# Optimization experiments

Measured on AMD Instinct MI355X. Metric: run time of the kernel, lower is better.

## Reference

```python
import jax, jax.numpy as jnp
import numpy as np


def _conv1x1(x, w, b=None):
    # x: (B, Cin, H, W), w: (Cout, Cin)
    y = jnp.einsum('oi,bihw->bohw', w, x)
    if b is not None:
        y = y + b[None, :, None, None]
    return y


def _adaptive_avg_pool(x, ps):
    # faithful torch AdaptiveAvgPool2d: bin i covers [floor(i*H/ps), ceil((i+1)*H/ps))
    H, W = x.shape[-2], x.shape[-1]
    rows = []
    for i in range(ps):
        hs, he = (i * H) // ps, -((-(i + 1) * H) // ps)
        cols = []
        for j in range(ps):
            ws, we = (j * W) // ps, -((-(j + 1) * W) // ps)
            cols.append(x[..., hs:he, ws:we].mean((-2, -1)))
        rows.append(jnp.stack(cols, -1))
    return jnp.stack(rows, -2)


def _bilinear(x, oh, ow, align_corners):
    H, W = x.shape[-2], x.shape[-1]
    def coords(o, I):
        if align_corners:
            c = jnp.arange(o, dtype=jnp.float32) * (float(I - 1) / max(o - 1, 1))
        else:
            c = jnp.clip((jnp.arange(o, dtype=jnp.float32) + 0.5) * (float(I) / o) - 0.5, 0.0, float(I - 1))
        i0 = jnp.floor(c).astype(jnp.int32)
        i1 = jnp.minimum(i0 + 1, I - 1)
        return i0, i1, (c - i0).astype(x.dtype)
    y0, y1, wy = coords(oh, H)
    x0, x1, wx = coords(ow, W)
    top = x[..., y0, :]
    bot = x[..., y1, :]
    a, b = top[..., x0], top[..., x1]
    c, d = bot[..., x0], bot[..., x1]
    r0 = a * (1 - wx) + b * wx
    r1 = c * (1 - wx) + d * wx
    return r0 * (1 - wy[:, None]) + r1 * wy[:, None]


def setup_inputs() -> dict:
    key = jax.random.key(0)
    ks = jax.random.split(key, 32)
    Cin, C, B, H, W = 512, 64, 2, 48, 48
    def rnd(k, shape, s=0.05):
        return jax.random.normal(k, shape, jnp.float32) * s
    inp = {
        'x': jax.random.normal(ks[0], (B, Cin, H, W), jnp.float32),
        'w_gc0': rnd(ks[1], (C, Cin)), 'b_gc0': rnd(ks[2], (C,)),
        'w_gc1': rnd(ks[3], (C, Cin)), 'b_gc1': rnd(ks[4], (C,)),
        'w_gc2': rnd(ks[5], (C, Cin)), 'b_gc2': rnd(ks[6], (C,)),
        'w_gc3': rnd(ks[7], (C, Cin)), 'b_gc3': rnd(ks[8], (C,)),
        'w_q': rnd(ks[9], (C // 8, C)), 'b_q': rnd(ks[10], (C // 8,)),
        'w_k': rnd(ks[11], (C // 8, C)), 'b_k': rnd(ks[12], (C // 8,)),
        'w_v': rnd(ks[13], (C, C)), 'b_v': rnd(ks[14], (C,)),
        'gamma': jnp.ones((1,), jnp.float32),
        'w_se1': rnd(ks[15], (C, C)), 'w_se2': rnd(ks[16], (C, C)),
        'w_se3': rnd(ks[17], (C, C)), 'w_se4': rnd(ks[18], (C, C)),
        'w_out0': rnd(ks[19], (256, 4 * C)), 'b_out0': rnd(ks[20], (256,)),
        'w_out1': rnd(ks[21], (128, 4 * C)), 'b_out1': rnd(ks[22], (128,)),
        'w_out2': rnd(ks[23], (64, 4 * C)), 'b_out2': rnd(ks[24], (64,)),
        'w_out3': rnd(ks[25], (64, 4 * C)), 'b_out3': rnd(ks[26], (64,)),
    }
    return inp


def reference(x, w_gc0, b_gc0, w_gc1, b_gc1, w_gc2, b_gc2, w_gc3, b_gc3,
              w_q, b_q, w_k, b_k, w_v, b_v, gamma,
              w_se1, w_se2, w_se3, w_se4,
              w_out0, b_out0, w_out1, b_out1, w_out2, b_out2, w_out3, b_out3):
    B, _, H, W = x.shape
    # multi-scale pooled branches (pool sizes 1,3,5), bilinear up w/ align_corners=True
    gcs = []
    for ps, w_, b_ in ((1, w_gc0, b_gc0), (3, w_gc1, b_gc1), (5, w_gc2, b_gc2)):
        p = jax.nn.relu(_conv1x1(_adaptive_avg_pool(x, ps), w_, b_))
        gcs.append(_bilinear(p, H, W, True))
    # full-resolution SA branch
    s = jax.nn.relu(_conv1x1(x, w_gc3, b_gc3))
    N = H * W
    q = _conv1x1(s, w_q, b_q).reshape(B, -1, N)   # (B, C/8, N)
    k = _conv1x1(s, w_k, b_k).reshape(B, -1, N)
    v = _conv1x1(s, w_v, b_v).reshape(B, -1, N)   # (B, C, N)
    attn = jax.nn.softmax(jnp.einsum('bcm,bcn->bmn', q, k), axis=-1)  # (B, N, N)
    sa = jnp.einsum('bcn,bmn->bcm', v, attn).reshape(s.shape)
    sa = gamma * sa + s
    # SE channel-attention weights (note original's cross pairing of branches)
    gap = lambda t: t.mean((2, 3), keepdims=True)
    y3 = _conv1x1(gap(gcs[0]), w_se4)
    y2 = _conv1x1(gap(gcs[1]), w_se3)
    y1 = _conv1x1(gap(gcs[2]), w_se2)
    y0 = _conv1x1(gap(sa), w_se1)
    wgt = jnp.concatenate([y0, y1, y2, y3], axis=2)      # (B, 64, 4, 1)
    wgt = jax.nn.softmax(jax.nn.sigmoid(wgt), axis=2)
    fused = jnp.concatenate([
        wgt[:, :, 0:1, :] * gcs[0],
        wgt[:, :, 1:2, :] * gcs[1],
        wgt[:, :, 2:3, :] * gcs[2],
        wgt[:, :, 3:4, :] * sa,
    ], axis=1)                                            # (B, 256, H, W)
    outs = []
    for sc, w_, b_ in ((2, w_out0, b_out0), (4, w_out1, b_out1), (8, w_out2, b_out2), (16, w_out3, b_out3)):
        y = jax.nn.relu(_conv1x1(fused, w_, b_))
        outs.append(_bilinear(y, H * sc, W * sc, False))  # nn.Upsample default align_corners=False
    return tuple(outs)
```

## Files before the change

### kernel.cpp

```cpp
#include <hip/hip_runtime.h>
#include <hip/hip_bf16.h>
#include <hip/hip_fp16.h>


typedef __attribute__((ext_vector_type(8))) short short8;
typedef __attribute__((ext_vector_type(4))) float f32x4;

#define GLOAD_LDS(gsrc, ldst) \
  __builtin_amdgcn_global_load_lds((const __attribute__((address_space(1))) void*)(gsrc), \
                                   (__attribute__((address_space(3))) void*)(ldst), 16, 0, 0)

static constexpr size_t OFF_P1 = 0;
static constexpr size_t OFF_P3 = OFF_P1 + 2*512;
static constexpr size_t OFF_P5 = OFF_P3 + 18*512;
static constexpr size_t OFF_G0 = OFF_P5 + 50*512;
static constexpr size_t OFF_G1 = OFF_G0 + 2*64;
static constexpr size_t OFF_G2 = OFF_G1 + 18*64;
static constexpr size_t OFF_S  = OFF_G2 + 50*64;
static constexpr size_t OFF_Q  = OFF_S  + 294912;
static constexpr size_t OFF_K  = OFF_Q  + 36864;
static constexpr size_t OFF_V  = OFF_K  + 36864;
static constexpr size_t OFF_SA = OFF_V  + 294912;
static constexpr size_t OFF_GC = OFF_SA + 294912;
static constexpr size_t OFF_MEAN = OFF_GC + 3*294912;
static constexpr size_t OFF_WGT  = OFF_MEAN + 512;
static constexpr size_t OFF_Y0 = OFF_WGT + 512;
static constexpr size_t OFF_Y1 = OFF_Y0 + 1179648;
static constexpr size_t OFF_Y2 = OFF_Y1 + 589824;
static constexpr size_t OFF_Y3 = OFF_Y2 + 294912;

__global__ __launch_bounds__(256) void k_pool(const float* __restrict__ x, float* __restrict__ wsp){
  __shared__ float pl[2304];
  __shared__ float red[4];
  int bc = blockIdx.x;
  int b = bc >> 9, cin = bc & 511;
  const float* src = x + (size_t)bc * 2304;
  int t = threadIdx.x;
  float ls = 0.f;
  #pragma unroll
  for (int j = 0; j < 9; j++){ int i = t + j*256; float v = src[i]; pl[i] = v; ls += v; }
  #pragma unroll
  for (int o = 32; o; o >>= 1) ls += __shfl_xor(ls, o);
  if ((t & 63) == 0) red[t >> 6] = ls;
  __syncthreads();
  if (t == 0) wsp[OFF_P1 + (size_t)b*512 + cin] = (red[0]+red[1]+red[2]+red[3]) * (1.f/2304.f);
  if (t < 9){
    int ry = t/3, rx = t%3; float sm = 0.f;
    for (int yy = 0; yy < 16; yy++)
      for (int xx = 0; xx < 16; xx++) sm += pl[(ry*16+yy)*48 + rx*16+xx];
    wsp[OFF_P3 + ((size_t)b*9 + t)*512 + cin] = sm * (1.f/256.f);
  } else if (t < 34){
    int j = t - 9; int ry = j/5, rx = j%5;
    int hs = (ry*48)/5, he = ((ry+1)*48+4)/5, cs = (rx*48)/5, ce = ((rx+1)*48+4)/5;
    float sm = 0.f;
    for (int yy = hs; yy < he; yy++)
      for (int xx = cs; xx < ce; xx++) sm += pl[yy*48+xx];
    wsp[OFF_P5 + ((size_t)b*25 + j)*512 + cin] = sm / (float)((he-hs)*(ce-cs));
  }
}

__global__ __launch_bounds__(256) void k_gcconv(
    const float* __restrict__ w0, const float* __restrict__ b0,
    const float* __restrict__ w1, const float* __restrict__ b1,
    const float* __restrict__ w2, const float* __restrict__ b2,
    float* __restrict__ wsp){
  int col = blockIdx.x;
  const float* w; const float* bias; const float* pool; float* dst;
  if (col < 2){ w = w0; bias = b0; pool = wsp + OFF_P1 + (size_t)col*512; dst = wsp + OFF_G0 + (size_t)col*64; }
  else if (col < 20){ int c = col-2;  w = w1; bias = b1; pool = wsp + OFF_P3 + (size_t)c*512; dst = wsp + OFF_G1 + (size_t)c*64; }
  else              { int c = col-20; w = w2; bias = b2; pool = wsp + OFF_P5 + (size_t)c*512; dst = wsp + OFF_G2 + (size_t)c*64; }
  int t = threadIdx.x; int r = t >> 2, qd = t & 3;
  const float* wr = w + (size_t)r*512 + qd*128;
  const float* pr = pool + qd*128;
  float acc = 0.f;
  #pragma unroll 8
  for (int k = 0; k < 128; k += 4){
    float4 wv = *(const float4*)(wr + k); float4 pv = *(const float4*)(pr + k);
    acc += wv.x*pv.x + wv.y*pv.y + wv.z*pv.z + wv.w*pv.w;
  }
  acc += __shfl_xor(acc, 1); acc += __shfl_xor(acc, 2);
  if (qd == 0) dst[r] = fmaxf(acc + bias[r], 0.f);
}

__global__ __launch_bounds__(256) void k_sgemm_qkv(const float* __restrict__ x,
    const float* __restrict__ w, const float* __restrict__ bias,
    const float* __restrict__ wq, const float* __restrict__ bq,
    const float* __restrict__ wk, const float* __restrict__ bk,
    const float* __restrict__ wv, const float* __restrict__ bv,
    float* __restrict__ wsp){
  __shared__ __align__(16) float wt[64][66];
  __shared__ __align__(16) float xs[64][32];
  __shared__ __align__(16) float s_lds[64][36];
  __shared__ float wq_lds[80][64];
  __shared__ float bqkv[80];
  int cb = blockIdx.x;
  int b = cb / 72, hw0 = (cb - b*72)*32;
  int tid = threadIdx.x;
  int wv_ = tid >> 6, lane = tid & 63;
  for (int i = tid; i < 5120; i += 256){
    int row = i >> 6, k = i & 63;
    wq_lds[row][k] = (row < 8) ? wq[(size_t)row*64 + k]
                   : (row < 16) ? wk[(size_t)(row-8)*64 + k]
                                : wv[(size_t)(row-16)*64 + k];
  }
  if (tid < 80) bqkv[tid] = (tid < 8) ? bq[tid] : (tid < 16) ? bk[tid-8] : bv[tid-16];
  int sr = tid >> 2, sseg = tid & 3;
  int cc0 = (tid & 7)*4, r0 = (tid >> 3)*2;
  const float* xb = x + (size_t)b*512*2304 + hw0;
  float acc[2][4] = {};
  for (int kc = 0; kc < 512; kc += 64){
    __syncthreads();
    {
      int rr0 = wv_*16 + (lane >> 3);
      const float* g0 = xb + (size_t)(kc + rr0)*2304 + (lane & 7)*4;
      const float* g1 = xb + (size_t)(kc + rr0 + 8)*2304 + (lane & 7)*4;
      GLOAD_LDS(g0, &xs[wv_*16][0]);
      GLOAD_LDS(g1, &xs[wv_*16 + 8][0]);
    }
    #pragma unroll
    for (int i = 0; i < 16; i += 4){
      float4 v = *(const float4*)(w + (size_t)sr*512 + kc + sseg*16 + i);
      wt[sseg*16+i+0][sr]=v.x; wt[sseg*16+i+1][sr]=v.y;
      wt[sseg*16+i+2][sr]=v.z; wt[sseg*16+i+3][sr]=v.w;
    }
    __syncthreads();
    #pragma unroll 4
    for (int k = 0; k < 64; k++){
      float2 wv2 = *(const float2*)&wt[k][r0];
      float4 xv = *(const float4*)&xs[k][cc0];
      acc[0][0]+=wv2.x*xv.x; acc[0][1]+=wv2.x*xv.y; acc[0][2]+=wv2.x*xv.z; acc[0][3]+=wv2.x*xv.w;
      acc[1][0]+=wv2.y*xv.x; acc[1][1]+=wv2.y*xv.y; acc[1][2]+=wv2.y*xv.z; acc[1][3]+=wv2.y*xv.w;
    }
  }
  #pragma unroll
  for (int i = 0; i < 2; i++){
    float bi = bias[r0+i];
    float4 o;
    o.x = fmaxf(acc[i][0]+bi, 0.f); o.y = fmaxf(acc[i][1]+bi, 0.f);
    o.z = fmaxf(acc[i][2]+bi, 0.f); o.w = fmaxf(acc[i][3]+bi, 0.f);
    *(float4*)(wsp + OFF_S + ((size_t)b*64 + r0+i)*2304 + hw0 + cc0) = o;
    *(float4*)&s_lds[r0+i][cc0] = o;
  }
  __syncthreads();
  int col = tid & 31, rgrp = tid >> 5;
  float a2[10];
  #pragma unroll
  for (int i = 0; i < 10; i++) a2[i] = bqkv[rgrp*10 + i];
  for (int k = 0; k < 64; k++){
    float sv = s_lds[k][col];
    #pragma unroll
    for (int i = 0; i < 10; i++) a2[i] += wq_lds[rgrp*10 + i][k]*sv;
  }
  __hip_bfloat16* Vb = reinterpret_cast<__hip_bfloat16*>(wsp + OFF_V);
  int hw = hw0 + col;
  #pragma unroll
  for (int i = 0; i < 10; i++){
    int r = rgrp*10 + i;
    if (r < 8)       wsp[OFF_Q + (size_t)b*18432 + (size_t)r*2304 + hw] = a2[i];
    else if (r < 16) wsp[OFF_K + (size_t)b*18432 + (size_t)(r-8)*2304 + hw] = a2[i];
    else             Vb[(size_t)b*147456 + (size_t)(r-16)*2304 + hw] = __float2bfloat16(a2[i]);
  }
}

__global__ __launch_bounds__(256) void k_attn(float* __restrict__ wsp, const float* __restrict__ gamma){
  int mb = blockIdx.x * 16;
  int b  = blockIdx.y;
  int t = threadIdx.x;
  int w = t >> 6, lane = t & 63;
  int arow = lane & 15, kg = lane >> 4;
  __shared__ float qs[16][8];
  __shared__ __align__(16) unsigned short plds[16][2312];
  __shared__ float redM[4][16], redS[4][16];
  __shared__ float tile[16][68];
  const float* Qp = wsp + OFF_Q + (size_t)b*18432;
  const float* Kp = wsp + OFF_K + (size_t)b*18432;
  if (t < 128) qs[t>>3][t&7] = Qp[(size_t)(t&7)*2304 + mb + (t>>3)];
  __syncthreads();
  float k8[9][8];
  #pragma unroll
  for (int j = 0; j < 9; j++){
    int n = j*256 + t;
    #pragma unroll
    for (int c = 0; c < 8; c++) k8[j][c] = Kp[(size_t)c*2304 + n];
  }
  float mx[16], ssum[16];
  #pragma unroll
  for (int m = 0; m < 16; m++){
    float q0=qs[m][0], q1=qs[m][1], q2=qs[m][2], q3=qs[m][3];
    float q4=qs[m][4], q5=qs[m][5], q6=qs[m][6], q7=qs[m][7];
    float lmx = -1e30f, ls = 0.f;
    #pragma unroll
    for (int j = 0; j < 9; j++){
      float l = q0*k8[j][0]+q1*k8[j][1]+q2*k8[j][2]+q3*k8[j][3]
              + q4*k8[j][4]+q5*k8[j][5]+q6*k8[j][6]+q7*k8[j][7];
      __half hv = __float2half(l);
      plds[m][j*256 + t] = __half_as_ushort(hv);
      float mo = lmx;
      lmx = fmaxf(lmx, l);
      ls = ls*__expf(mo - lmx) + __expf(l - lmx);
    }
    mx[m] = lmx; ssum[m] = ls;
  }
  #pragma unroll
  for (int m = 0; m < 16; m++){
    float M = mx[m], S = ssum[m];
    #pragma unroll
    for (int off = 32; off; off >>= 1){
      float oM = __shfl_xor(M, off), oS = __shfl_xor(S, off);
      float nM = fmaxf(M, oM);
      S = S*__expf(M - nM) + oS*__expf(oM - nM);
      M = nM;
    }
    if (lane == 0){ redM[w][m] = M; redS[w][m] = S; }
  }
  __syncthreads();
  float Mf[16], invS[16];
  #pragma unroll
  for (int m = 0; m < 16; m++){
    float M0 = redM[0][m], M1 = redM[1][m], M2 = redM[2][m], M3 = redM[3][m];
    float M = fmaxf(fmaxf(M0, M1), fmaxf(M2, M3));
    float S = redS[0][m]*__expf(M0-M) + redS[1][m]*__expf(M1-M)
            + redS[2][m]*__expf(M2-M) + redS[3][m]*__expf(M3-M);
    Mf[m] = M; invS[m] = 1.f/S;
  }
  const short* Vb = (const short*)(wsp + OFF_V) + (size_t)b*147456 + (size_t)(w*16 + arow)*2304;
  f32x4 acc = {0.f, 0.f, 0.f, 0.f};
  for (int j = 0; j < 9; j++){
    int n = j*256 + t;
    #pragma unroll
    for (int m = 0; m < 16; m++){
      float l = __half2float(__ushort_as_half(plds[m][n]));
      float p = __expf(l - Mf[m]) * invS[m];
      __hip_bfloat16 pb = __float2bfloat16(p);
      plds[m][n] = *(unsigned short*)&pb;
    }
    __syncthreads();
    #pragma unroll
    for (int ks = 0; ks < 8; ks++){
      int nb = j*256 + ks*32 + kg*8;
      short8 a  = *(const short8*)&plds[arow][nb];
      short8 bv = *(const short8*)(Vb + nb);
      acc = __builtin_amdgcn_mfma_f32_16x16x32_bf16(a, bv, acc, 0, 0, 0);
    }
  }
  #pragma unroll
  for (int r = 0; r < 4; r++) tile[kg*4 + r][w*16 + arow] = acc[r];
  __syncthreads();
  int c = t >> 2, mq = t & 3;
  float g = gamma[0];
  const float* Sp = wsp + OFF_S + (size_t)b*147456 + (size_t)c*2304 + mb + mq*4;
  float4 s4 = *(const float4*)Sp;
  float4 o;
  o.x = g*tile[mq*4+0][c] + s4.x;
  o.y = g*tile[mq*4+1][c] + s4.y;
  o.z = g*tile[mq*4+2][c] + s4.z;
  o.w = g*tile[mq*4+3][c] + s4.w;
  *(float4*)(wsp + OFF_SA + (size_t)b*147456 + (size_t)c*2304 + mb + mq*4) = o;
}

__device__ void gcup_body(int u, float* __restrict__ wsp){
  int px = (u % 9)*256 + threadIdx.x;
  int pb = u / 9;
  int c = pb & 63, b = (pb >> 6) & 1, t = pb >> 7;
  int oy = px / 48, ox = px - oy*48;
  int ps; const float* g;
  if (t == 0){ ps = 1; g = wsp + OFF_G0 + (size_t)b*64; }
  else if (t == 1){ ps = 3; g = wsp + OFF_G1 + (size_t)b*9*64; }
  else { ps = 5; g = wsp + OFF_G2 + (size_t)b*25*64; }
  float scale = (ps - 1) / 47.f;
  float cy = oy*scale, cx = ox*scale;
  int y0 = (int)cy, x0 = (int)cx;
  float wy = cy - y0, wx = cx - x0;
  int y1 = min(y0+1, ps-1), x1 = min(x0+1, ps-1);
  float a  = g[(y0*ps+x0)*64 + c], bq = g[(y0*ps+x1)*64 + c];
  float cc = g[(y1*ps+x0)*64 + c], d  = g[(y1*ps+x1)*64 + c];
  float v = (a*(1.f-wx) + bq*wx)*(1.f-wy) + (cc*(1.f-wx) + d*wx)*wy;
  wsp[OFF_GC + (((size_t)t*2 + b)*64 + c)*2304 + px] = v;
}

__device__ void gap_body(int blk, float* __restrict__ wsp){
  __shared__ float red[4];
  int c = blk & 63, b = blk >> 6;
  const float* src = wsp + OFF_SA + ((size_t)b*64 + c)*2304;
  float s = 0.f;
  for (int i = threadIdx.x; i < 2304; i += 256) s += src[i];
  #pragma unroll
  for (int o = 32; o; o >>= 1) s += __shfl_xor(s, o);
  if ((threadIdx.x & 63) == 0) red[threadIdx.x >> 6] = s;
  __syncthreads();
  if (threadIdx.x == 0)
    wsp[OFF_MEAN + (size_t)b*64 + c] = (red[0]+red[1]+red[2]+red[3]) * (1.f/2304.f);
}

__global__ __launch_bounds__(256) void k_gcup_gap(float* __restrict__ wsp){
  int bx = blockIdx.x;
  if (bx < 3456) gcup_body(bx, wsp);
  else           gap_body(bx - 3456, wsp);
}

__global__ __launch_bounds__(256) void k_se(
    const float* __restrict__ w_se1, const float* __restrict__ w_se2,
    const float* __restrict__ w_se3, const float* __restrict__ w_se4,
    float* __restrict__ wsp){
  int b = blockIdx.x; int tid = threadIdx.x;
  int g = tid >> 6, c = tid & 63;
  __shared__ float mean_lds[4][64];
  float mv;
  if (g == 0){
    mv = wsp[OFF_MEAN + (size_t)b*64 + c];
  } else if (g == 3){
    mv = wsp[OFF_G0 + (size_t)b*64 + c];
  } else if (g == 2){
    float w3[3] = {0.f,0.f,0.f};
    for (int o = 0; o < 48; o++){
      float cc = o*(2.f/47.f); int i0 = (int)cc; float f = cc - i0;
      int i1 = min(i0+1, 2);
      w3[i0] += 1.f - f; w3[i1] += f;
    }
    float s = 0.f;
    for (int sy = 0; sy < 3; sy++)
      for (int sx = 0; sx < 3; sx++)
        s += w3[sy]*w3[sx]*wsp[OFF_G1 + ((size_t)b*9 + sy*3 + sx)*64 + c];
    mv = s * (1.f/(48.f*48.f));
  } else {
    float w5[5] = {0.f,0.f,0.f,0.f,0.f};
    for (int o = 0; o < 48; o++){
      float cc = o*(4.f/47.f); int i0 = (int)cc; float f = cc - i0;
      int i1 = min(i0+1, 4);
      w5[i0] += 1.f - f; w5[i1] += f;
    }
    float s = 0.f;
    for (int sy = 0; sy < 5; sy++)
      for (int sx = 0; sx < 5; sx++)
        s += w5[sy]*w5[sx]*wsp[OFF_G2 + ((size_t)b*25 + sy*5 + sx)*64 + c];
    mv = s * (1.f/(48.f*48.f));
  }
  mean_lds[g][c] = mv;
  __syncthreads();
  const float* w = (g == 0) ? w_se1 : (g == 1) ? w_se2 : (g == 2) ? w_se3 : w_se4;
  float acc = 0.f;
  for (int j = 0; j < 64; j++) acc += w[(size_t)c*64 + j]*mean_lds[g][j];
  float sg = 1.f / (1.f + __expf(-acc));
  __shared__ float sh[4][64];
  sh[g][c] = sg;
  __syncthreads();
  float a0 = sh[0][c], a1 = sh[1][c], a2 = sh[2][c], a3 = sh[3][c];
  float mxv = fmaxf(fmaxf(a0, a1), fmaxf(a2, a3));
  float e = __expf(sg - mxv);
  float sum = __expf(a0-mxv) + __expf(a1-mxv) + __expf(a2-mxv) + __expf(a3-mxv);
  wsp[OFF_WGT + ((size_t)b*4 + g)*64 + c] = e / sum;
}

__global__ __launch_bounds__(256) void k_outgemm(
    const float* __restrict__ w0, const float* __restrict__ b0,
    const float* __restrict__ w1, const float* __restrict__ b1,
    const float* __restrict__ w2, const float* __restrict__ b2,
    const float* __restrict__ w3, const float* __restrict__ b3,
    float* __restrict__ wsp){
  __shared__ __align__(16) float wt[64][68];
  __shared__ __align__(16) float xsh[64][64];
  __shared__ float wg[256];
  int cb = blockIdx.x, rb = blockIdx.y;
  int b = cb / 36, hw0 = (cb - b*36)*64;
  const float* wsrc; const float* bsrc; size_t dstoff; int dstC; int row0;
  if (rb < 4){ wsrc = w0 + (size_t)rb*64*256; bsrc = b0 + rb*64; dstoff = OFF_Y0; dstC = 256; row0 = rb*64; }
  else if (rb < 6){ wsrc = w1 + (size_t)(rb-4)*64*256; bsrc = b1 + (rb-4)*64; dstoff = OFF_Y1; dstC = 128; row0 = (rb-4)*64; }
  else if (rb == 6){ wsrc = w2; bsrc = b2; dstoff = OFF_Y2; dstC = 64; row0 = 0; }
  else { wsrc = w3; bsrc = b3; dstoff = OFF_Y3; dstC = 64; row0 = 0; }
  int tid = threadIdx.x;
  int wv_ = tid >> 6, lane = tid & 63;
  wg[tid] = wsp[OFF_WGT + (size_t)b*256 + tid];
  int sr = tid >> 2, sseg = tid & 3;
  int cc0 = (tid & 15)*4, r0 = (tid >> 4)*4;
  float acc[4][4] = {};
  for (int kc = 0; kc < 256; kc += 64){
    __syncthreads();
    {
      int gidx = kc >> 6;
      size_t srcbase = (gidx < 3) ? OFF_GC + ((size_t)(gidx*2 + b))*147456
                                  : OFF_SA + (size_t)b*147456;
      const float* gb = wsp + srcbase + hw0 + (lane & 15)*4;
      int rr = wv_*16 + (lane >> 4);
      #pragma unroll
      for (int i = 0; i < 4; i++)
        GLOAD_LDS(gb + (size_t)(rr + i*4)*2304, &xsh[wv_*16 + i*4][0]);
    }
    #pragma unroll
    for (int i = 0; i < 16; i += 4){
      float4 v = *(const float4*)(wsrc + (size_t)sr*256 + kc + sseg*16 + i);
      int kl = sseg*16 + i;
      wt[kl+0][sr]=v.x*wg[kc+kl+0]; wt[kl+1][sr]=v.y*wg[kc+kl+1];
      wt[kl+2][sr]=v.z*wg[kc+kl+2]; wt[kl+3][sr]=v.w*wg[kc+kl+3];
    }
    __syncthreads();
    #pragma unroll 4
    for (int k = 0; k < 64; k++){
      float4 wv = *(const float4*)&wt[k][r0];
      float4 xv = *(const float4*)&xsh[k][cc0];
      acc[0][0]+=wv.x*xv.x; acc[0][1]+=wv.x*xv.y; acc[0][2]+=wv.x*xv.z; acc[0][3]+=wv.x*xv.w;
      acc[1][0]+=wv.y*xv.x; acc[1][1]+=wv.y*xv.y; acc[1][2]+=wv.y*xv.z; acc[1][3]+=wv.y*xv.w;
      acc[2][0]+=wv.z*xv.x; acc[2][1]+=wv.z*xv.y; acc[2][2]+=wv.z*xv.z; acc[2][3]+=wv.z*xv.w;
      acc[3][0]+=wv.w*xv.x; acc[3][1]+=wv.w*xv.y; acc[3][2]+=wv.w*xv.z; acc[3][3]+=wv.w*xv.w;
    }
  }
  #pragma unroll
  for (int i = 0; i < 4; i++){
    float bi = bsrc[r0+i];
    float4 o;
    o.x = fmaxf(acc[i][0]+bi, 0.f); o.y = fmaxf(acc[i][1]+bi, 0.f);
    o.z = fmaxf(acc[i][2]+bi, 0.f); o.w = fmaxf(acc[i][3]+bi, 0.f);
    *(float4*)(wsp + dstoff + ((size_t)b*dstC + row0 + r0 + i)*2304 + hw0 + cc0) = o;
  }
}

template<int SC>
__device__ __forceinline__ void up_one(int idx, const float* __restrict__ src, float* __restrict__ dst){
  constexpr int OW = 48*SC, OH = 48*SC;
  constexpr int WQ = OW/4;
  int q = idx % WQ; int rest = idx / WQ;
  int oy = rest % OH; int pc = rest / OH;
  const float* sp = src + (size_t)pc * 2304;
  float cy = fminf(fmaxf((oy + 0.5f)*(1.0f/SC) - 0.5f, 0.f), 47.f);
  int y0 = (int)cy;
  float wy = cy - y0;
  int y1 = min(y0+1, 47);
  const float* r0 = sp + y0*48; const float* r1 = sp + y1*48;
  float outv[4];
  #pragma unroll
  for (int i = 0; i < 4; i++){
    int ox = q*4 + i;
    float cx = fminf(fmaxf((ox + 0.5f)*(1.0f/SC) - 0.5f, 0.f), 47.f);
    int x0 = (int)cx; float wx = cx - x0; int x1 = min(x0+1, 47);
    float a  = r0[x0]*(1.f-wx) + r0[x1]*wx;
    float bq = r1[x0]*(1.f-wx) + r1[x1]*wx;
    outv[i] = a*(1.f-wy) + bq*wy;
  }
  f32x4 o; o[0] = outv[0]; o[1] = outv[1]; o[2] = outv[2]; o[3] = outv[3];
  f32x4* dp = (f32x4*)(dst + (size_t)pc*OH*OW + (size_t)oy*OW + q*4);
  __builtin_nontemporal_store(o, dp);
}

__global__ __launch_bounds__(256) void k_upsample_all(const float* __restrict__ wsp, float* __restrict__ out){
  int t = blockIdx.x*256 + threadIdx.x;
  if (t < 1179648)       up_one<2>(t,           wsp + OFF_Y0, out);
  else if (t < 3538944)  up_one<4>(t - 1179648, wsp + OFF_Y1, out + 4718592);
  else if (t < 8257536)  up_one<8>(t - 3538944, wsp + OFF_Y2, out + 14155776);
  else                   up_one<16>(t - 8257536, wsp + OFF_Y3, out + 33030144);
}

extern "C" void kernel_launch(void* const* d_in, const int* in_sizes, int n_in,
                              void* d_out, int out_size, void* d_ws, size_t ws_size,
                              hipStream_t stream){
  const float* x     = (const float*)d_in[0];
  const float* w_gc0 = (const float*)d_in[1];
  const float* b_gc0 = (const float*)d_in[2];
  const float* w_gc1 = (const float*)d_in[3];
  const float* b_gc1 = (const float*)d_in[4];
  const float* w_gc2 = (const float*)d_in[5];
  const float* b_gc2 = (const float*)d_in[6];
  const float* w_gc3 = (const float*)d_in[7];
  const float* b_gc3 = (const float*)d_in[8];
  const float* w_q   = (const float*)d_in[9];
  const float* b_q   = (const float*)d_in[10];
  const float* w_k   = (const float*)d_in[11];
  const float* b_k   = (const float*)d_in[12];
  const float* w_v   = (const float*)d_in[13];
  const float* b_v   = (const float*)d_in[14];
  const float* gamma = (const float*)d_in[15];
  const float* w_se1 = (const float*)d_in[16];
  const float* w_se2 = (const float*)d_in[17];
  const float* w_se3 = (const float*)d_in[18];
  const float* w_se4 = (const float*)d_in[19];
  const float* w_out0 = (const float*)d_in[20];
  const float* b_out0 = (const float*)d_in[21];
  const float* w_out1 = (const float*)d_in[22];
  const float* b_out1 = (const float*)d_in[23];
  const float* w_out2 = (const float*)d_in[24];
  const float* b_out2 = (const float*)d_in[25];
  const float* w_out3 = (const float*)d_in[26];
  const float* b_out3 = (const float*)d_in[27];
  float* wsp = (float*)d_ws;
  float* out = (float*)d_out;

  k_pool     <<<1024, 256, 0, stream>>>(x, wsp);
  k_gcconv   <<<70,   256, 0, stream>>>(w_gc0,b_gc0,w_gc1,b_gc1,w_gc2,b_gc2, wsp);
  k_sgemm_qkv<<<144,  256, 0, stream>>>(x, w_gc3, b_gc3, w_q,b_q,w_k,b_k,w_v,b_v, wsp);
  k_attn     <<<dim3(144,2), 256, 0, stream>>>(wsp, gamma);
  k_gcup_gap <<<3584, 256, 0, stream>>>(wsp);
  k_se       <<<2,    256, 0, stream>>>(w_se1,w_se2,w_se3,w_se4, wsp);
  k_outgemm  <<<dim3(72,8), 256, 0, stream>>>(w_out0,b_out0,w_out1,b_out1,w_out2,b_out2,w_out3,b_out3, wsp);
  k_upsample_all<<<105984, 256, 0, stream>>>(wsp, out);
}
```

Before: 215.1 us.

## Stage upsample source rows in LDS and process output row bands per block

The bilinear upsample kernel is restructured so each block handles a band of output rows for one channel plane. The needed source rows are staged once into shared memory, and each thread then produces three float4 outputs. The intent is to cut redundant global/L2 reads of source pixels and to reduce block count and per-thread index overhead in a store-bound kernel. The cost is an extra __syncthreads per block and more complex band/row bookkeeping, with clamping in case a band needs more rows than NR.

```diff
diff --git a/kernel.cpp b/kernel.cpp
--- a/kernel.cpp
+++ b/kernel.cpp
@@ -413,39 +413,56 @@
   }
 }
 
-template<int SC>
-__device__ __forceinline__ void up_one(int idx, const float* __restrict__ src, float* __restrict__ dst){
-  constexpr int OW = 48*SC, OH = 48*SC;
-  constexpr int WQ = OW/4;
-  int q = idx % WQ; int rest = idx / WQ;
-  int oy = rest % OH; int pc = rest / OH;
+template<int SC, int RPB, int NR>
+__device__ __forceinline__ void up_band(int bi, const float* __restrict__ src,
+                                        float* __restrict__ dst, float (*srow)[48]){
+  constexpr int OW = 48*SC, OH = 48*SC, OW4 = OW/4;
+  constexpr float inv = 1.0f/SC;
+  constexpr int BANDS = OH/RPB;
+  int pc = bi / BANDS, band = bi - pc*BANDS;
+  int r0b = band * RPB;
   const float* sp = src + (size_t)pc * 2304;
-  float cy = fminf(fmaxf((oy + 0.5f)*(1.0f/SC) - 0.5f, 0.f), 47.f);
-  int y0 = (int)cy;
-  float wy = cy - y0;
-  int y1 = min(y0+1, 47);
-  const float* r0 = sp + y0*48; const float* r1 = sp + y1*48;
-  float outv[4];
-  #pragma unroll
-  for (int i = 0; i < 4; i++){
-    int ox = q*4 + i;
-    float cx = fminf(fmaxf((ox + 0.5f)*(1.0f/SC) - 0.5f, 0.f), 47.f);
-    int x0 = (int)cx; float wx = cx - x0; int x1 = min(x0+1, 47);
-    float a  = r0[x0]*(1.f-wx) + r0[x1]*wx;
-    float bq = r1[x0]*(1.f-wx) + r1[x1]*wx;
-    outv[i] = a*(1.f-wy) + bq*wy;
-  }
-  f32x4 o; o[0] = outv[0]; o[1] = outv[1]; o[2] = outv[2]; o[3] = outv[3];
-  f32x4* dp = (f32x4*)(dst + (size_t)pc*OH*OW + (size_t)oy*OW + q*4);
-  __builtin_nontemporal_store(o, dp);
+  int y0min = (int)fmaxf((r0b + 0.5f)*inv - 0.5f, 0.f);
+  int t = threadIdx.x;
+  for (int i = t; i < NR*48; i += 256){
+    int r = i / 48, cc = i - r*48;
+    srow[r][cc] = sp[min(y0min + r, 47)*48 + cc];
+  }
+  __syncthreads();
+  float* dbase = dst + (size_t)pc*OH*OW + (size_t)r0b*OW;
+  #pragma unroll
+  for (int p = 0; p < 3; p++){
+    int local = p*256 + t;
+    int lrow = local / OW4;
+    int q = local - lrow*OW4;
+    int oy = r0b + lrow;
+    float cy = fminf(fmaxf((oy + 0.5f)*inv - 0.5f, 0.f), 47.f);
+    int y0 = (int)cy; float wy = cy - y0;
+    int y1 = min(y0 + 1, 47);
+    const float* s0 = srow[min(y0 - y0min, NR-1)];
+    const float* s1 = srow[min(y1 - y0min, NR-1)];
+    float ov[4];
+    #pragma unroll
+    for (int i = 0; i < 4; i++){
+      float cx = fminf(fmaxf((q*4 + i + 0.5f)*inv - 0.5f, 0.f), 47.f);
+      int x0 = (int)cx; float wx = cx - x0;
+      int x1 = min(x0 + 1, 47);
+      float a = s0[x0] + (s0[x1] - s0[x0])*wx;
+      float b = s1[x0] + (s1[x1] - s1[x0])*wx;
+      ov[i] = a + (b - a)*wy;
+    }
+    f32x4 o; o[0]=ov[0]; o[1]=ov[1]; o[2]=ov[2]; o[3]=ov[3];
+    __builtin_nontemporal_store(o, (f32x4*)(dbase + (size_t)local*4));
+  }
 }
 
 __global__ __launch_bounds__(256) void k_upsample_all(const float* __restrict__ wsp, float* __restrict__ out){
-  int t = blockIdx.x*256 + threadIdx.x;
-  if (t < 1179648)       up_one<2>(t,           wsp + OFF_Y0, out);
-  else if (t < 3538944)  up_one<4>(t - 1179648, wsp + OFF_Y1, out + 4718592);
-  else if (t < 8257536)  up_one<8>(t - 3538944, wsp + OFF_Y2, out + 14155776);
-  else                   up_one<16>(t - 8257536, wsp + OFF_Y3, out + 33030144);
+  __shared__ float srow[18][48];
+  int b = blockIdx.x;
+  if (b < 1536)        up_band<2,32,18>(b,         wsp + OFF_Y0, out,            srow);
+  else if (b < 4608)   up_band<4,16,6> (b - 1536,  wsp + OFF_Y1, out + 4718592,  srow);
+  else if (b < 10752)  up_band<8,8,3>  (b - 4608,  wsp + OFF_Y2, out + 14155776, srow);
+  else                 up_band<16,4,3> (b - 10752, wsp + OFF_Y3, out + 33030144, srow);
 }
 
 extern "C" void kernel_launch(void* const* d_in, const int* in_sizes, int n_in,
@@ -489,5 +506,5 @@
   k_gcup_gap <<<3584, 256, 0, stream>>>(wsp);
   k_se       <<<2,    256, 0, stream>>>(w_se1,w_se2,w_se3,w_se4, wsp);
   k_outgemm  <<<dim3(72,8), 256, 0, stream>>>(w_out0,b_out0,w_out1,b_out1,w_out2,b_out2,w_out3,b_out3, wsp);
-  k_upsample_all<<<105984, 256, 0, stream>>>(wsp, out);
-}
+  k_upsample_all<<<35328, 256, 0, stream>>>(wsp, out);
+}
```

Result: faster. 193.4 us (-10.1%).
